# Kernel tuning notes

Hardware: AMD Instinct MI355X
Metric: run time of the kernel (lower is better)

The kernel has to match this reference:

```python
import jax, jax.numpy as jnp
import numpy as np

DIM = 512
INNER = 512        # heads(8) * dim_head(64)
OUT_DIM = 256
SCALE = 64 ** -0.5  # dim_head ** -0.5
BN_EPS = 1e-5


def setup_inputs() -> dict:
    key = jax.random.key(0)
    ks = jax.random.split(key, 8)
    B, H, W = 2, 96, 320
    return {
        "left_feat": jax.random.normal(ks[0], (B, DIM, H, W), jnp.float32),
        "right_feat": jax.random.normal(ks[1], (B, DIM, H, W), jnp.float32),
        "wq": jax.random.normal(ks[2], (INNER, DIM), jnp.float32) * (DIM ** -0.5),
        "wk": jax.random.normal(ks[3], (INNER, DIM), jnp.float32) * (DIM ** -0.5),
        "wv": jax.random.normal(ks[4], (INNER, DIM), jnp.float32) * (DIM ** -0.5),
        "w1": jax.random.normal(ks[5], (OUT_DIM, INNER * 2), jnp.float32) * ((INNER * 2) ** -0.5),
        "bn_gamma": jnp.ones((OUT_DIM,), jnp.float32),
        "bn_beta": jnp.zeros((OUT_DIM,), jnp.float32),
        "bn_mean": jnp.zeros((OUT_DIM,), jnp.float32),
        "bn_var": jnp.ones((OUT_DIM,), jnp.float32),
        "w2": jax.random.normal(ks[6], (OUT_DIM, OUT_DIM), jnp.float32) * (OUT_DIM ** -0.5),
    }


def reference(left_feat, right_feat, wq, wk, wv, w1, bn_gamma, bn_beta, bn_mean, bn_var, w2):
    # conv1x1 projections, directly producing channels-last [b, h, w, c]
    q = jnp.einsum('bchw,oc->bhwo', left_feat, wq)
    k = jnp.einsum('bchw,oc->bhwo', right_feat, wk)
    v = jnp.einsum('bchw,oc->bhwo', right_feat, wv)
    # cross-attention along width, independently per (batch, row)
    dots = jnp.einsum('bhwc,bhxc->bhwx', q, k) * SCALE   # [b, h, w, w]
    attn = jax.nn.softmax(dots, axis=-1)
    out = jnp.einsum('bhwx,bhxc->bhwc', attn, v)         # [b, h, w, c]
    out = out.transpose(0, 3, 1, 2)                      # [b, c, h, w]
    new_left = jnp.concatenate([left_feat, out], axis=1)  # [b, 2*inner, h, w]
    # to_out: conv1x1 -> BN (eval mode, running stats) -> LeakyReLU(0.2) -> conv1x1
    y = jnp.einsum('bchw,oc->bohw', new_left, w1)
    inv = jax.lax.rsqrt(bn_var + BN_EPS)
    y = (y - bn_mean[None, :, None, None]) * (inv * bn_gamma)[None, :, None, None] \
        + bn_beta[None, :, None, None]
    y = jnp.where(y >= 0, y, 0.2 * y)
    return jnp.einsum('bchw,oc->bohw', y, w2)
```

## Files before the change

### kernel.cpp

```cpp
#include <hip/hip_runtime.h>

typedef __bf16 bf16x8 __attribute__((ext_vector_type(8)));
typedef float f32x4 __attribute__((ext_vector_type(4)));
typedef unsigned short u16x8 __attribute__((ext_vector_type(8)));

#define MFMA16(a, b, c) __builtin_amdgcn_mfma_f32_16x16x32_bf16((a), (b), (c), 0, 0, 0)
#define GLOAD_LDS(gp, lp) __builtin_amdgcn_global_load_lds( \
    (const __attribute__((address_space(1))) void*)(uintptr_t)(const void*)(gp), \
    (__attribute__((address_space(3))) void*)(uintptr_t)(void*)(lp), 16, 0, 0)

#define NB 2
#define NC 512
#define NH 96
#define NW 320
#define PH 30720
#define NPIX 61440
#define NOUT 256

__device__ __forceinline__ unsigned short f2bf(float f) {
    union { float f; unsigned u; } v; v.f = f;
    unsigned r = v.u + 0x7fffu + ((v.u >> 16) & 1u);
    return (unsigned short)(r >> 16);
}

__global__ void k_cast(const float* __restrict__ src, unsigned short* __restrict__ dst, int n) {
    int i = blockIdx.x * 256 + threadIdx.x;
    if (i < n) dst[i] = f2bf(src[i]);
}

__global__ __launch_bounds__(256) void k_transpose(
        const float* __restrict__ L, const float* __restrict__ R,
        unsigned short* __restrict__ Lcl, unsigned short* __restrict__ Rcl) {
    __shared__ float t[64][65];
    int z = blockIdx.z;
    int b = z & 1, which = z >> 1;
    const float* src = which ? R : L;
    unsigned short* dst = which ? Rcl : Lcl;
    int c0 = blockIdx.y * 64;
    int p0 = blockIdx.x * 64;
    int tt = threadIdx.x;

    int cl4 = tt >> 4;
    int px = (tt & 15) * 4;
#pragma unroll
    for (int i = 0; i < 4; ++i) {
        int cl = i * 16 + cl4;
        f32x4 v = *reinterpret_cast<const f32x4*>(src + (size_t)(b * NC + c0 + cl) * PH + p0 + px);
        t[cl][px + 0] = v[0];
        t[cl][px + 1] = v[1];
        t[cl][px + 2] = v[2];
        t[cl][px + 3] = v[3];
    }
    __syncthreads();

    int cc = (tt & 7) * 8;
    int pl0 = tt >> 3;
#pragma unroll
    for (int j = 0; j < 2; ++j) {
        int pl = j * 32 + pl0;
        u16x8 ov;
#pragma unroll
        for (int i = 0; i < 8; ++i) ov[i] = f2bf(t[cc + i][pl]);
        *reinterpret_cast<u16x8*>(dst + (size_t)(b * PH + p0 + pl) * NC + c0 + cc) = ov;
    }
}

template <int MODE>
__global__ __launch_bounds__(256) void k_gemm(
        const unsigned short* __restrict__ A0,
        const unsigned short* __restrict__ A1,
        const unsigned short* __restrict__ Bb,
        unsigned short* __restrict__ Dbf,
        float* __restrict__ Df32,
        const float* __restrict__ g, const float* __restrict__ be,
        const float* __restrict__ mu, const float* __restrict__ va) {
    constexpr int SA = (MODE == 4) ? NOUT : NC;
    constexpr int SB = (MODE == 3) ? 1024 : (MODE == 4) ? NOUT : NC;
    constexpr int KS = (MODE == 3) ? 32 : (MODE == 4) ? 8 : 16;
    constexpr int NTO = (MODE <= 2) ? 4 : 2;
    constexpr int TOT = 480 * NTO;

    __shared__ unsigned short Asm[2][128 * 32];
    __shared__ unsigned short Bsm[2][128 * 32];

    int pphys = blockIdx.x;
    int lgc = (pphys & 7) * (TOT / 8) + (pphys >> 3);
    int pixt = lgc / NTO, ot = lgc % NTO;
    const int mbase = ((MODE == 2 || MODE == 4) ? ot : pixt) * 128;
    const int nbase = ((MODE == 2 || MODE == 4) ? pixt : ot) * 128;

    const int lane = threadIdx.x & 63, w = threadIdx.x >> 6;
    const int lr = lane & 15, lg = lane >> 4;
    const int wr = w >> 1, wc = w & 1;

    auto stageA = [&](int buf, int kc) {
        const unsigned short* srcA = A0;
        int colOff = kc * 32;
        if constexpr (MODE == 3) {
            if (kc >= 16) { srcA = A1; colOff = (kc - 16) * 32; }
        }
#pragma unroll
        for (int j = 0; j < 2; ++j) {
            int cb = w * 128 + j * 64;
            int c = cb + lane;
            const unsigned short* gp = srcA + (size_t)(mbase + (c >> 2)) * SA + colOff + (c & 3) * 8;
            GLOAD_LDS(gp, Asm[buf] + cb * 8);
        }
    };
    auto stageB = [&](int buf, int kc) {
#pragma unroll
        for (int j = 0; j < 2; ++j) {
            int cb = w * 128 + j * 64;
            int c = cb + lane;
            const unsigned short* gp = Bb + (size_t)(nbase + (c >> 2)) * SB + kc * 32 + (c & 3) * 8;
            GLOAD_LDS(gp, Bsm[buf] + cb * 8);
        }
    };

    f32x4 acc[4][4] = {};

    stageA(0, 0);
    stageB(0, 0);
    __syncthreads();

    for (int kc = 0; kc < KS; ++kc) {
        int cur = kc & 1;
        if (kc + 1 < KS) {
            stageA(cur ^ 1, kc + 1);
            stageB(cur ^ 1, kc + 1);
        }
        bf16x8 af[4], bfr[4];
#pragma unroll
        for (int i = 0; i < 4; ++i)
            af[i] = *reinterpret_cast<const bf16x8*>(Asm[cur] + (wr * 64 + i * 16 + lr) * 32 + lg * 8);
#pragma unroll
        for (int j = 0; j < 4; ++j)
            bfr[j] = *reinterpret_cast<const bf16x8*>(Bsm[cur] + (wc * 64 + j * 16 + lr) * 32 + lg * 8);
        __builtin_amdgcn_s_setprio(1);
#pragma unroll
        for (int i = 0; i < 4; ++i)
#pragma unroll
            for (int j = 0; j < 4; ++j)
                acc[i][j] = MFMA16(af[i], bfr[j], acc[i][j]);
        __builtin_amdgcn_s_setprio(0);
        __syncthreads();
    }

    const int lr4 = lg * 4;
    if constexpr (MODE <= 1) {
#pragma unroll
        for (int i = 0; i < 4; ++i)
#pragma unroll
            for (int j = 0; j < 4; ++j) {
                int ocol = nbase + wc * 64 + j * 16 + lr;
#pragma unroll
                for (int r = 0; r < 4; ++r) {
                    int prow = mbase + wr * 64 + i * 16 + lr4 + r;
                    Dbf[(size_t)prow * NC + ocol] = f2bf(acc[i][j][r]);
                }
            }
    } else if constexpr (MODE == 2) {
#pragma unroll
        for (int i = 0; i < 4; ++i)
#pragma unroll
            for (int j = 0; j < 4; ++j) {
                int pix = nbase + wc * 64 + j * 16 + lr;
                int b = pix / PH, ph = pix % PH;
                int hh = ph / NW, x = ph % NW;
#pragma unroll
                for (int r = 0; r < 4; ++r) {
                    int crow = mbase + wr * 64 + i * 16 + lr4 + r;
                    Dbf[((size_t)(b * NH + hh) * NC + crow) * NW + x] = f2bf(acc[i][j][r]);
                }
            }
    } else if constexpr (MODE == 3) {
#pragma unroll
        for (int j = 0; j < 4; ++j) {
            int o = nbase + wc * 64 + j * 16 + lr;
            float sc = g[o] * rsqrtf(va[o] + 1e-5f);
            float sh = be[o] - mu[o] * sc;
#pragma unroll
            for (int i = 0; i < 4; ++i)
#pragma unroll
                for (int r = 0; r < 4; ++r) {
                    int prow = mbase + wr * 64 + i * 16 + lr4 + r;
                    float y = acc[i][j][r] * sc + sh;
                    y = (y >= 0.f) ? y : 0.2f * y;
                    Dbf[(size_t)prow * NOUT + o] = f2bf(y);
                }
        }
    } else {
#pragma unroll
        for (int j = 0; j < 4; ++j) {
            int pix = nbase + wc * 64 + j * 16 + lr;
            int b = pix / PH, ph = pix % PH;
#pragma unroll
            for (int i = 0; i < 4; ++i)
#pragma unroll
                for (int r = 0; r < 4; ++r) {
                    int o = mbase + wr * 64 + i * 16 + lr4 + r;
                    Df32[((size_t)b * NOUT + o) * PH + ph] = acc[i][j][r];
                }
        }
    }
}

__global__ __launch_bounds__(256, 2) void k_attn(
        const unsigned short* __restrict__ Q, const unsigned short* __restrict__ K,
        const unsigned short* __restrict__ Vt, unsigned short* __restrict__ O) {
    __shared__ unsigned short P[64][328];
    __shared__ unsigned short KV[32 * 512];

    int pphys = blockIdx.x;
    int l = (pphys & 7) * 120 + (pphys >> 3);
    int head = l / 5, qt = l % 5;
    int b = head / NH, hh = head % NH;
    int lane = threadIdx.x & 63, w = threadIdx.x >> 6;
    int lr = lane & 15, lg = lane >> 4;
    int rowbase = b * PH + hh * NW;
    int qrow = rowbase + qt * 64 + w * 16 + lr;

    bf16x8 qf[16];
#pragma unroll
    for (int kc = 0; kc < 16; ++kc)
        qf[kc] = *reinterpret_cast<const bf16x8*>(Q + (size_t)qrow * NC + kc * 32 + lg * 8);

    f32x4 acc[20];
#pragma unroll
    for (int xt = 0; xt < 20; ++xt) acc[xt] = f32x4{0.f, 0.f, 0.f, 0.f};

    u16x8 kreg[4];
    auto kload = [&](int t) {
#pragma unroll
        for (int j = 0; j < 4; ++j) {
            int r = w * 4 + j;
            kreg[j] = *reinterpret_cast<const u16x8*>(
                K + (size_t)(rowbase + t * 16 + r) * NC + ((lane ^ (r & 7)) * 8));
        }
    };
    auto kwrite = [&](int buf) {
#pragma unroll
        for (int j = 0; j < 4; ++j) {
            int r = w * 4 + j;
            *reinterpret_cast<u16x8*>(KV + (buf * 16 + r) * 512 + lane * 8) = kreg[j];
        }
    };

    kload(0);
    kwrite(0);
    __syncthreads();
#pragma unroll
    for (int t = 0; t < 20; ++t) {
        if (t + 1 < 20) kload(t + 1);
        int buf = t & 1;
        int rsw = lr & 7;
        __builtin_amdgcn_s_setprio(1);
#pragma unroll
        for (int kc = 0; kc < 16; ++kc) {
            bf16x8 kf = *reinterpret_cast<const bf16x8*>(
                KV + (buf * 16 + lr) * 512 + (((kc * 4 + lg) ^ rsw) * 8));
            acc[t] = MFMA16(qf[kc], kf, acc[t]);
        }
        __builtin_amdgcn_s_setprio(0);
        __syncthreads();
        if (t + 1 < 20) kwrite(buf ^ 1);
        __syncthreads();
    }

    int vbase = (b * NH + hh) * NC;
    u16x8 vreg[8];
    auto vload = [&](int s) {
#pragma unroll
        for (int j = 0; j < 8; ++j) {
            int c = (w * 8 + j) * 16 + (lane >> 2);
            int qg = (lane & 3) ^ ((lane >> 3) & 3);
            vreg[j] = *reinterpret_cast<const u16x8*>(
                Vt + (size_t)(vbase + c) * NW + s * 32 + qg * 8);
        }
    };
    auto vwrite = [&]() {
#pragma unroll
        for (int j = 0; j < 8; ++j)
            *reinterpret_cast<u16x8*>(KV + (w * 8 + j) * 512 + lane * 8) = vreg[j];
    };
    vload(0);

#pragma unroll
    for (int xt = 0; xt < 20; ++xt)
#pragma unroll
        for (int r = 0; r < 4; ++r) acc[xt][r] *= 0.125f;
    float m[4] = {-1e30f, -1e30f, -1e30f, -1e30f};
#pragma unroll
    for (int xt = 0; xt < 20; ++xt)
#pragma unroll
        for (int r = 0; r < 4; ++r) m[r] = fmaxf(m[r], acc[xt][r]);
#pragma unroll
    for (int mask = 1; mask < 16; mask <<= 1)
#pragma unroll
        for (int r = 0; r < 4; ++r) m[r] = fmaxf(m[r], __shfl_xor(m[r], mask));
    float s4[4] = {0.f, 0.f, 0.f, 0.f};
#pragma unroll
    for (int xt = 0; xt < 20; ++xt)
#pragma unroll
        for (int r = 0; r < 4; ++r) {
            float e = __expf(acc[xt][r] - m[r]);
            acc[xt][r] = e;
            s4[r] += e;
        }
#pragma unroll
    for (int mask = 1; mask < 16; mask <<= 1)
#pragma unroll
        for (int r = 0; r < 4; ++r) s4[r] += __shfl_xor(s4[r], mask);
#pragma unroll
    for (int xt = 0; xt < 20; ++xt)
#pragma unroll
        for (int r = 0; r < 4; ++r)
            P[w * 16 + lg * 4 + r][xt * 16 + lr] = f2bf(acc[xt][r]);
    __syncthreads();
    vwrite();
    __syncthreads();

    f32x4 oacc[32];
#pragma unroll
    for (int ct = 0; ct < 32; ++ct) oacc[ct] = f32x4{0.f, 0.f, 0.f, 0.f};

#pragma unroll
    for (int s = 0; s < 10; ++s) {
        if (s + 1 < 10) vload(s + 1);
        bf16x8 pf = *reinterpret_cast<const bf16x8*>(&P[w * 16 + lr][s * 32 + lg * 8]);
        __builtin_amdgcn_s_setprio(1);
#pragma unroll
        for (int ct = 0; ct < 32; ++ct) {
            bf16x8 vf = *reinterpret_cast<const bf16x8*>(
                KV + ct * 512 + lr * 32 + ((lg ^ ((lr >> 1) & 3)) * 8));
            oacc[ct] = MFMA16(pf, vf, oacc[ct]);
        }
        __builtin_amdgcn_s_setprio(0);
        __syncthreads();
        if (s + 1 < 10) vwrite();
        __syncthreads();
    }

#pragma unroll
    for (int ct = 0; ct < 32; ++ct)
#pragma unroll
        for (int r = 0; r < 4; ++r) {
            int prow = rowbase + qt * 64 + w * 16 + lg * 4 + r;
            O[(size_t)prow * NC + ct * 16 + lr] = f2bf(oacc[ct][r] / s4[r]);
        }
}

extern "C" void kernel_launch(void* const* d_in, const int* in_sizes, int n_in,
                              void* d_out, int out_size, void* d_ws, size_t ws_size,
                              hipStream_t stream) {
    const float* left  = (const float*)d_in[0];
    const float* right = (const float*)d_in[1];
    const float* wq = (const float*)d_in[2];
    const float* wk = (const float*)d_in[3];
    const float* wv = (const float*)d_in[4];
    const float* w1 = (const float*)d_in[5];
    const float* bn_g = (const float*)d_in[6];
    const float* bn_b = (const float*)d_in[7];
    const float* bn_m = (const float*)d_in[8];
    const float* bn_v = (const float*)d_in[9];
    const float* w2 = (const float*)d_in[10];
    float* out = (float*)d_out;

    size_t off = 0;
    auto alloc = [&](size_t bytes) -> void* {
        void* p = (char*)d_ws + off;
        off += (bytes + 255) & ~(size_t)255;
        return p;
    };
    const size_t clb = (size_t)NPIX * NC * 2;
    unsigned short* Lcl = (unsigned short*)alloc(clb);
    unsigned short* Rcl = (unsigned short*)alloc(clb);
    unsigned short* Qb  = (unsigned short*)alloc(clb);
    unsigned short* Kb  = (unsigned short*)alloc(clb);
    unsigned short* Vt  = (unsigned short*)alloc(clb);
    unsigned short* Wqb = (unsigned short*)alloc((size_t)NC * NC * 2);
    unsigned short* Wkb = (unsigned short*)alloc((size_t)NC * NC * 2);
    unsigned short* Wvb = (unsigned short*)alloc((size_t)NC * NC * 2);
    unsigned short* W1b = (unsigned short*)alloc((size_t)NOUT * 1024 * 2);
    unsigned short* W2b = (unsigned short*)alloc((size_t)NOUT * NOUT * 2);
    unsigned short* AO = Rcl;
    unsigned short* Yb = Qb;

    k_cast<<<dim3((NC * NC + 255) / 256), 256, 0, stream>>>(wq, Wqb, NC * NC);
    k_cast<<<dim3((NC * NC + 255) / 256), 256, 0, stream>>>(wk, Wkb, NC * NC);
    k_cast<<<dim3((NC * NC + 255) / 256), 256, 0, stream>>>(wv, Wvb, NC * NC);
    k_cast<<<dim3((NOUT * 1024 + 255) / 256), 256, 0, stream>>>(w1, W1b, NOUT * 1024);
    k_cast<<<dim3((NOUT * NOUT + 255) / 256), 256, 0, stream>>>(w2, W2b, NOUT * NOUT);

    k_transpose<<<dim3(PH / 64, NC / 64, 4), 256, 0, stream>>>(left, right, Lcl, Rcl);

    k_gemm<0><<<dim3(1920), 256, 0, stream>>>(Lcl, nullptr, Wqb, Qb, nullptr, nullptr, nullptr, nullptr, nullptr);
    k_gemm<1><<<dim3(1920), 256, 0, stream>>>(Rcl, nullptr, Wkb, Kb, nullptr, nullptr, nullptr, nullptr, nullptr);
    k_gemm<2><<<dim3(1920), 256, 0, stream>>>(Wvb, nullptr, Rcl, Vt, nullptr, nullptr, nullptr, nullptr, nullptr);

    k_attn<<<dim3(960), 256, 0, stream>>>(Qb, Kb, Vt, AO);

    k_gemm<3><<<dim3(960), 256, 0, stream>>>(Lcl, AO, W1b, Yb, nullptr, bn_g, bn_b, bn_m, bn_v);

    k_gemm<4><<<dim3(960), 256, 0, stream>>>(W2b, nullptr, Yb, nullptr, out, nullptr, nullptr, nullptr, nullptr);
}
```

Baseline: 406.7 us.

## Fold K and V projections into weights via associativity of attention matmuls

Precomputes Wq^T Wk (so scores become q'·r with q' = L·(Wk^T Wq) and raw right features as keys). It also folds Wv into W1's attention half (W1_attn·Wv), so attention outputs weighted sums of raw right features. This removes the separate K and V projection GEMMs and the V transpose store. The transpose kernel additionally emits a channel-major bf16 copy of the right features for use as V. The cost is small weight-product GEMMs plus an extra full-size bf16 write of R, and rounding the combined weights to bf16 adds some precision risk.

```diff
diff --git a/kernel.cpp b/kernel.cpp
--- a/kernel.cpp
+++ b/kernel.cpp
@@ -3,6 +3,7 @@
 typedef __bf16 bf16x8 __attribute__((ext_vector_type(8)));
 typedef float f32x4 __attribute__((ext_vector_type(4)));
 typedef unsigned short u16x8 __attribute__((ext_vector_type(8)));
+typedef unsigned short u16x4 __attribute__((ext_vector_type(4)));
 
 #define MFMA16(a, b, c) __builtin_amdgcn_mfma_f32_16x16x32_bf16((a), (b), (c), 0, 0, 0)
 #define GLOAD_LDS(gp, lp) __builtin_amdgcn_global_load_lds( \
@@ -28,9 +29,39 @@
     if (i < n) dst[i] = f2bf(src[i]);
 }
 
+__global__ __launch_bounds__(256) void k_wtrans(
+        const float* __restrict__ wq, const float* __restrict__ wk, const float* __restrict__ wv,
+        unsigned short* __restrict__ WqT, unsigned short* __restrict__ WkT, unsigned short* __restrict__ WvT) {
+    __shared__ float t[64][65];
+    int z = blockIdx.z;
+    const float* src = (z == 0) ? wq : (z == 1) ? wk : wv;
+    unsigned short* dst = (z == 0) ? WqT : (z == 1) ? WkT : WvT;
+    int i0 = blockIdx.y * 64;
+    int c0 = blockIdx.x * 64;
+    int tt = threadIdx.x;
+    int r4 = tt >> 4, px = (tt & 15) * 4;
+#pragma unroll
+    for (int i = 0; i < 4; ++i) {
+        int il = i * 16 + r4;
+        f32x4 v = *reinterpret_cast<const f32x4*>(src + (size_t)(i0 + il) * 512 + c0 + px);
+        t[il][px + 0] = v[0]; t[il][px + 1] = v[1]; t[il][px + 2] = v[2]; t[il][px + 3] = v[3];
+    }
+    __syncthreads();
+    int cc = (tt & 7) * 8, pl0 = tt >> 3;
+#pragma unroll
+    for (int j = 0; j < 2; ++j) {
+        int pl = j * 32 + pl0;
+        u16x8 ov;
+#pragma unroll
+        for (int i = 0; i < 8; ++i) ov[i] = f2bf(t[cc + i][pl]);
+        *reinterpret_cast<u16x8*>(dst + (size_t)(c0 + pl) * 512 + i0 + cc) = ov;
+    }
+}
+
 __global__ __launch_bounds__(256) void k_transpose(
         const float* __restrict__ L, const float* __restrict__ R,
-        unsigned short* __restrict__ Lcl, unsigned short* __restrict__ Rcl) {
+        unsigned short* __restrict__ Lcl, unsigned short* __restrict__ Rcl,
+        unsigned short* __restrict__ Rbf) {
     __shared__ float t[64][65];
     int z = blockIdx.z;
     int b = z & 1, which = z >> 1;
@@ -50,6 +81,12 @@
         t[cl][px + 1] = v[1];
         t[cl][px + 2] = v[2];
         t[cl][px + 3] = v[3];
+        if (which) {
+            u16x4 sv;
+#pragma unroll
+            for (int k = 0; k < 4; ++k) sv[k] = f2bf(v[k]);
+            *reinterpret_cast<u16x4*>(Rbf + (size_t)(b * NC + c0 + cl) * PH + p0 + px) = sv;
+        }
     }
     __syncthreads();
 
@@ -70,15 +107,17 @@
         const unsigned short* __restrict__ A0,
         const unsigned short* __restrict__ A1,
         const unsigned short* __restrict__ Bb,
+        const unsigned short* __restrict__ Bb2,
         unsigned short* __restrict__ Dbf,
         float* __restrict__ Df32,
         const float* __restrict__ g, const float* __restrict__ be,
         const float* __restrict__ mu, const float* __restrict__ va) {
-    constexpr int SA = (MODE == 4) ? NOUT : NC;
+    constexpr int SA = (MODE == 4) ? NOUT : (MODE == 6) ? 1024 : NC;
+    constexpr int AOFF = (MODE == 6) ? 512 : 0;
     constexpr int SB = (MODE == 3) ? 1024 : (MODE == 4) ? NOUT : NC;
     constexpr int KS = (MODE == 3) ? 32 : (MODE == 4) ? 8 : 16;
-    constexpr int NTO = (MODE <= 2) ? 4 : 2;
-    constexpr int TOT = 480 * NTO;
+    constexpr int NTO = (MODE == 3 || MODE == 4) ? 2 : 4;
+    constexpr int TOT = (MODE == 5) ? 16 : (MODE == 6) ? 8 : ((MODE == 3 || MODE == 4) ? 960 : 1920);
 
     __shared__ unsigned short Asm[2][128 * 32];
     __shared__ unsigned short Bsm[2][128 * 32];
@@ -86,8 +125,8 @@
     int pphys = blockIdx.x;
     int lgc = (pphys & 7) * (TOT / 8) + (pphys >> 3);
     int pixt = lgc / NTO, ot = lgc % NTO;
-    const int mbase = ((MODE == 2 || MODE == 4) ? ot : pixt) * 128;
-    const int nbase = ((MODE == 2 || MODE == 4) ? pixt : ot) * 128;
+    const int mbase = ((MODE == 4) ? ot : pixt) * 128;
+    const int nbase = ((MODE == 4) ? pixt : ot) * 128;
 
     const int lane = threadIdx.x & 63, w = threadIdx.x >> 6;
     const int lr = lane & 15, lg = lane >> 4;
@@ -103,16 +142,22 @@
         for (int j = 0; j < 2; ++j) {
             int cb = w * 128 + j * 64;
             int c = cb + lane;
-            const unsigned short* gp = srcA + (size_t)(mbase + (c >> 2)) * SA + colOff + (c & 3) * 8;
+            const unsigned short* gp = srcA + (size_t)(mbase + (c >> 2)) * SA + AOFF + colOff + (c & 3) * 8;
             GLOAD_LDS(gp, Asm[buf] + cb * 8);
         }
     };
     auto stageB = [&](int buf, int kc) {
+        const unsigned short* srcB = Bb;
+        int colOff = kc * 32;
+        int sb = SB;
+        if constexpr (MODE == 3) {
+            if (kc >= 16) { srcB = Bb2; colOff = (kc - 16) * 32; sb = 512; }
+        }
 #pragma unroll
         for (int j = 0; j < 2; ++j) {
             int cb = w * 128 + j * 64;
             int c = cb + lane;
-            const unsigned short* gp = Bb + (size_t)(nbase + (c >> 2)) * SB + kc * 32 + (c & 3) * 8;
+            const unsigned short* gp = srcB + (size_t)(nbase + (c >> 2)) * sb + colOff + (c & 3) * 8;
             GLOAD_LDS(gp, Bsm[buf] + cb * 8);
         }
     };
@@ -147,7 +192,7 @@
     }
 
     const int lr4 = lg * 4;
-    if constexpr (MODE <= 1) {
+    if constexpr (MODE == 0 || MODE >= 5) {
 #pragma unroll
         for (int i = 0; i < 4; ++i)
 #pragma unroll
@@ -157,20 +202,6 @@
                 for (int r = 0; r < 4; ++r) {
                     int prow = mbase + wr * 64 + i * 16 + lr4 + r;
                     Dbf[(size_t)prow * NC + ocol] = f2bf(acc[i][j][r]);
-                }
-            }
-    } else if constexpr (MODE == 2) {
-#pragma unroll
-        for (int i = 0; i < 4; ++i)
-#pragma unroll
-            for (int j = 0; j < 4; ++j) {
-                int pix = nbase + wc * 64 + j * 16 + lr;
-                int b = pix / PH, ph = pix % PH;
-                int hh = ph / NW, x = ph % NW;
-#pragma unroll
-                for (int r = 0; r < 4; ++r) {
-                    int crow = mbase + wr * 64 + i * 16 + lr4 + r;
-                    Dbf[((size_t)(b * NH + hh) * NC + crow) * NW + x] = f2bf(acc[i][j][r]);
                 }
             }
     } else if constexpr (MODE == 3) {
@@ -207,7 +238,7 @@
 
 __global__ __launch_bounds__(256, 2) void k_attn(
         const unsigned short* __restrict__ Q, const unsigned short* __restrict__ K,
-        const unsigned short* __restrict__ Vt, unsigned short* __restrict__ O) {
+        const unsigned short* __restrict__ Vb, unsigned short* __restrict__ O) {
     __shared__ unsigned short P[64][328];
     __shared__ unsigned short KV[32 * 512];
 
@@ -267,7 +298,6 @@
         __syncthreads();
     }
 
-    int vbase = (b * NH + hh) * NC;
     u16x8 vreg[8];
     auto vload = [&](int s) {
 #pragma unroll
@@ -275,7 +305,7 @@
             int c = (w * 8 + j) * 16 + (lane >> 2);
             int qg = (lane & 3) ^ ((lane >> 3) & 3);
             vreg[j] = *reinterpret_cast<const u16x8*>(
-                Vt + (size_t)(vbase + c) * NW + s * 32 + qg * 8);
+                Vb + (size_t)(b * NC + c) * PH + hh * NW + s * 32 + qg * 8);
         }
     };
     auto vwrite = [&]() {
@@ -375,32 +405,33 @@
     const size_t clb = (size_t)NPIX * NC * 2;
     unsigned short* Lcl = (unsigned short*)alloc(clb);
     unsigned short* Rcl = (unsigned short*)alloc(clb);
+    unsigned short* Rbf = (unsigned short*)alloc(clb);
     unsigned short* Qb  = (unsigned short*)alloc(clb);
-    unsigned short* Kb  = (unsigned short*)alloc(clb);
-    unsigned short* Vt  = (unsigned short*)alloc(clb);
-    unsigned short* Wqb = (unsigned short*)alloc((size_t)NC * NC * 2);
-    unsigned short* Wkb = (unsigned short*)alloc((size_t)NC * NC * 2);
-    unsigned short* Wvb = (unsigned short*)alloc((size_t)NC * NC * 2);
+    unsigned short* Ub  = (unsigned short*)alloc(clb);
+    unsigned short* WqT = (unsigned short*)alloc((size_t)NC * NC * 2);
+    unsigned short* WkT = (unsigned short*)alloc((size_t)NC * NC * 2);
+    unsigned short* WvT = (unsigned short*)alloc((size_t)NC * NC * 2);
+    unsigned short* Mt  = (unsigned short*)alloc((size_t)NC * NC * 2);
+    unsigned short* WX  = (unsigned short*)alloc((size_t)NOUT * NC * 2);
     unsigned short* W1b = (unsigned short*)alloc((size_t)NOUT * 1024 * 2);
     unsigned short* W2b = (unsigned short*)alloc((size_t)NOUT * NOUT * 2);
-    unsigned short* AO = Rcl;
     unsigned short* Yb = Qb;
 
-    k_cast<<<dim3((NC * NC + 255) / 256), 256, 0, stream>>>(wq, Wqb, NC * NC);
-    k_cast<<<dim3((NC * NC + 255) / 256), 256, 0, stream>>>(wk, Wkb, NC * NC);
-    k_cast<<<dim3((NC * NC + 255) / 256), 256, 0, stream>>>(wv, Wvb, NC * NC);
     k_cast<<<dim3((NOUT * 1024 + 255) / 256), 256, 0, stream>>>(w1, W1b, NOUT * 1024);
     k_cast<<<dim3((NOUT * NOUT + 255) / 256), 256, 0, stream>>>(w2, W2b, NOUT * NOUT);
 
-    k_transpose<<<dim3(PH / 64, NC / 64, 4), 256, 0, stream>>>(left, right, Lcl, Rcl);
-
-    k_gemm<0><<<dim3(1920), 256, 0, stream>>>(Lcl, nullptr, Wqb, Qb, nullptr, nullptr, nullptr, nullptr, nullptr);
-    k_gemm<1><<<dim3(1920), 256, 0, stream>>>(Rcl, nullptr, Wkb, Kb, nullptr, nullptr, nullptr, nullptr, nullptr);
-    k_gemm<2><<<dim3(1920), 256, 0, stream>>>(Wvb, nullptr, Rcl, Vt, nullptr, nullptr, nullptr, nullptr, nullptr);
-
-    k_attn<<<dim3(960), 256, 0, stream>>>(Qb, Kb, Vt, AO);
-
-    k_gemm<3><<<dim3(960), 256, 0, stream>>>(Lcl, AO, W1b, Yb, nullptr, bn_g, bn_b, bn_m, bn_v);
-
-    k_gemm<4><<<dim3(960), 256, 0, stream>>>(W2b, nullptr, Yb, nullptr, out, nullptr, nullptr, nullptr, nullptr);
-}
+    k_wtrans<<<dim3(8, 8, 3), 256, 0, stream>>>(wq, wk, wv, WqT, WkT, WvT);
+
+    k_transpose<<<dim3(PH / 64, NC / 64, 4), 256, 0, stream>>>(left, right, Lcl, Rcl, Rbf);
+
+    k_gemm<5><<<dim3(16), 256, 0, stream>>>(WkT, nullptr, WqT, nullptr, Mt, nullptr, nullptr, nullptr, nullptr, nullptr);
+    k_gemm<6><<<dim3(8), 256, 0, stream>>>(W1b, nullptr, WvT, nullptr, WX, nullptr, nullptr, nullptr, nullptr, nullptr);
+
+    k_gemm<0><<<dim3(1920), 256, 0, stream>>>(Lcl, nullptr, Mt, nullptr, Qb, nullptr, nullptr, nullptr, nullptr, nullptr);
+
+    k_attn<<<dim3(960), 256, 0, stream>>>(Qb, Rcl, Rbf, Ub);
+
+    k_gemm<3><<<dim3(960), 256, 0, stream>>>(Lcl, Ub, W1b, WX, Yb, nullptr, bn_g, bn_b, bn_m, bn_v);
+
+    k_gemm<4><<<dim3(960), 256, 0, stream>>>(W2b, nullptr, Yb, nullptr, nullptr, out, nullptr, nullptr, nullptr, nullptr);
+}
```

Result: faster. 353.3 us (median of 2 runs) (-13.1%).
